# Performance work log

Measured on AMD Instinct MI355X. Metric: run time of the kernel, lower is better.

The kernel has to match this reference:

```python
import jax, jax.numpy as jnp
import numpy as np

B, T, IN, H, OUT = 128, 256, 1, 5000, 20


def setup_inputs() -> dict:
    key = jax.random.key(0)
    k1, k2, k3, k4, k5 = jax.random.split(key, 5)
    return {
        "x": jax.random.normal(k1, (B, T, IN), dtype=jnp.float32),
        "W_in": jax.random.normal(k2, (H, IN), dtype=jnp.float32) * (1.0 / np.sqrt(IN)),
        "b_in": jax.random.normal(k3, (H,), dtype=jnp.float32) * 0.01,
        "W_out": jax.random.normal(k4, (OUT, H), dtype=jnp.float32) * (1.0 / np.sqrt(H)),
        "b_out": jax.random.normal(k5, (OUT,), dtype=jnp.float32) * 0.01,
    }


def reference(x, W_in, b_in, W_out, b_out):
    # x: [B, T, IN]; recurrence: h_{t+1} = tanh(x_t @ W_in^T + b_in + h_t)
    batch = x.shape[0]
    hidden = W_in.shape[0]
    h0 = jnp.zeros((batch, hidden), dtype=x.dtype)
    xs = jnp.swapaxes(x, 0, 1)  # [T, B, IN] for scan over time

    def step(h, x_t):
        h_new = jnp.tanh(x_t @ W_in.T + b_in + h)
        return h_new, None

    h_final, _ = jax.lax.scan(step, h0, xs)
    logits = h_final @ W_out.T + b_out  # [B, OUT]
    return jax.nn.softmax(logits, axis=-1)
```

## Files before the change

kernel.cpp:

```cpp
#include <hip/hip_runtime.h>

#define T_STEPS 256
#define BATCH   128
#define HIDDEN  5000
#define NOUT    20
#define HB      256

__global__ __launch_bounds__(256, 8)
void rnn_recurrence(const float* __restrict__ x,
                    const float* __restrict__ W_in,
                    const float* __restrict__ b_in,
                    float* __restrict__ h_out) {
    __shared__ float xs[T_STEPS];
    const int hb  = blockIdx.x;
    const int b   = blockIdx.y;
    const int tid = threadIdx.x;

    xs[tid] = x[b * T_STEPS + tid];
    __syncthreads();

    const int hidx = hb * HB + tid;
    if (hidx < HIDDEN) {
        const float c     = 2.8853900817779268f;
        const float inv_c = 0.34657359027997264f;
        const float wc = W_in[hidx] * c;
        const float bc = b_in[hidx] * c;
        float hc = 0.0f;
        #pragma unroll 8
        for (int t = 0; t < T_STEPS; ++t) {
            float u = fmaf(xs[t], wc, hc + bc);
            float e = __builtin_amdgcn_exp2f(u);
            float r = __builtin_amdgcn_rcpf(e + 1.0f);
            hc = fmaf(-2.0f * c, r, c);
        }
        h_out[b * HIDDEN + hidx] = hc * inv_c;
    }
}

__global__ __launch_bounds__(256)
void head_softmax(const float* __restrict__ h,
                  const float* __restrict__ W_out,
                  const float* __restrict__ b_out,
                  float* __restrict__ out) {
    const int b   = blockIdx.x;
    const int tid = threadIdx.x;

    float acc[NOUT];
    #pragma unroll
    for (int o = 0; o < NOUT; ++o) acc[o] = 0.0f;

    for (int i = tid; i < HIDDEN; i += 256) {
        const float hv = h[b * HIDDEN + i];
        #pragma unroll
        for (int o = 0; o < NOUT; ++o)
            acc[o] = fmaf(hv, W_out[o * HIDDEN + i], acc[o]);
    }

    #pragma unroll
    for (int o = 0; o < NOUT; ++o) {
        #pragma unroll
        for (int s = 32; s > 0; s >>= 1)
            acc[o] += __shfl_down(acc[o], s, 64);
    }

    __shared__ float partial[4][NOUT];
    const int wid = tid >> 6, lane = tid & 63;
    if (lane == 0) {
        #pragma unroll
        for (int o = 0; o < NOUT; ++o) partial[wid][o] = acc[o];
    }
    __syncthreads();

    if (tid == 0) {
        float logits[NOUT];
        float m = -1e30f;
        #pragma unroll
        for (int o = 0; o < NOUT; ++o) {
            float v = partial[0][o] + partial[1][o] + partial[2][o]
                    + partial[3][o] + b_out[o];
            logits[o] = v;
            m = fmaxf(m, v);
        }
        float s = 0.0f;
        float e[NOUT];
        #pragma unroll
        for (int o = 0; o < NOUT; ++o) {
            e[o] = __builtin_amdgcn_exp2f((logits[o] - m) * 1.4426950408889634f);
            s += e[o];
        }
        const float inv = 1.0f / s;
        #pragma unroll
        for (int o = 0; o < NOUT; ++o) out[b * NOUT + o] = e[o] * inv;
    }
}

extern "C" void kernel_launch(void* const* d_in, const int* in_sizes, int n_in,
                              void* d_out, int out_size, void* d_ws, size_t ws_size,
                              hipStream_t stream) {
    const float* x     = (const float*)d_in[0];
    const float* W_in  = (const float*)d_in[1];
    const float* b_in  = (const float*)d_in[2];
    const float* W_out = (const float*)d_in[3];
    const float* b_out = (const float*)d_in[4];
    float* out  = (float*)d_out;
    float* h_ws = (float*)d_ws;

    dim3 grid1((HIDDEN + HB - 1) / HB, BATCH);
    rnn_recurrence<<<grid1, 256, 0, stream>>>(x, W_in, b_in, h_ws);
    head_softmax<<<BATCH, 256, 0, stream>>>(h_ws, W_out, b_out, out);
}
```

Before: 110.4 us.

## Process two hidden units per thread, fold bias into exp, vectorize head loads

Each thread now runs two independent recurrences, which gives more instruction-level parallelism to hide the exp2/rcp latency on the serial dependency chain and halves the grid. The bias is folded algebraically into a precomputed multiplier exp2(b*c), so the per-step add becomes part of an fma. The shared-memory staging of x is replaced by direct global (cached) reads. The head kernel uses float4 loads for h and W_out. Per-step precision may shift slightly because exp2(u)*K replaces exp2(u+bc), which can overflow differently for large arguments.

```diff
diff --git a/kernel.cpp b/kernel.cpp
--- a/kernel.cpp
+++ b/kernel.cpp
@@ -3,38 +3,47 @@
 #define T_STEPS 256
 #define BATCH   128
 #define HIDDEN  5000
+#define NHALF   2500
 #define NOUT    20
-#define HB      256
 
-__global__ __launch_bounds__(256, 8)
+__global__ __launch_bounds__(256)
 void rnn_recurrence(const float* __restrict__ x,
                     const float* __restrict__ W_in,
                     const float* __restrict__ b_in,
                     float* __restrict__ h_out) {
-    __shared__ float xs[T_STEPS];
-    const int hb  = blockIdx.x;
-    const int b   = blockIdx.y;
-    const int tid = threadIdx.x;
+    const int b  = blockIdx.y;
+    const int i0 = blockIdx.x * 256 + threadIdx.x;
+    if (i0 >= NHALF) return;
+    const int i1 = i0 + NHALF;
 
-    xs[tid] = x[b * T_STEPS + tid];
-    __syncthreads();
+    const float c     = 2.8853900817779268f;
+    const float inv_c = 0.34657359027997264f;
+    const float n2c   = -5.7707801635558537f;
 
-    const int hidx = hb * HB + tid;
-    if (hidx < HIDDEN) {
-        const float c     = 2.8853900817779268f;
-        const float inv_c = 0.34657359027997264f;
-        const float wc = W_in[hidx] * c;
-        const float bc = b_in[hidx] * c;
-        float hc = 0.0f;
-        #pragma unroll 8
-        for (int t = 0; t < T_STEPS; ++t) {
-            float u = fmaf(xs[t], wc, hc + bc);
-            float e = __builtin_amdgcn_exp2f(u);
-            float r = __builtin_amdgcn_rcpf(e + 1.0f);
-            hc = fmaf(-2.0f * c, r, c);
-        }
-        h_out[b * HIDDEN + hidx] = hc * inv_c;
+    const float wc0 = W_in[i0] * c;
+    const float wc1 = W_in[i1] * c;
+    const float K0  = __builtin_amdgcn_exp2f(b_in[i0] * c);
+    const float K1  = __builtin_amdgcn_exp2f(b_in[i1] * c);
+
+    const float* __restrict__ xrow = x + b * T_STEPS;
+
+    float hc0 = 0.0f, hc1 = 0.0f;
+    #pragma unroll 16
+    for (int t = 0; t < T_STEPS; ++t) {
+        const float xv = xrow[t];
+        float u0 = fmaf(xv, wc0, hc0);
+        float u1 = fmaf(xv, wc1, hc1);
+        float e0 = __builtin_amdgcn_exp2f(u0);
+        float e1 = __builtin_amdgcn_exp2f(u1);
+        float d0 = fmaf(e0, K0, 1.0f);
+        float d1 = fmaf(e1, K1, 1.0f);
+        float r0 = __builtin_amdgcn_rcpf(d0);
+        float r1 = __builtin_amdgcn_rcpf(d1);
+        hc0 = fmaf(r0, n2c, c);
+        hc1 = fmaf(r1, n2c, c);
     }
+    h_out[b * HIDDEN + i0] = hc0 * inv_c;
+    h_out[b * HIDDEN + i1] = hc1 * inv_c;
 }
 
 __global__ __launch_bounds__(256)
@@ -45,15 +54,23 @@
     const int b   = blockIdx.x;
     const int tid = threadIdx.x;
 
+    const float4* __restrict__ h4 = (const float4*)(h + b * HIDDEN);
+    const float4* __restrict__ w4 = (const float4*)W_out;
+
     float acc[NOUT];
     #pragma unroll
     for (int o = 0; o < NOUT; ++o) acc[o] = 0.0f;
 
-    for (int i = tid; i < HIDDEN; i += 256) {
-        const float hv = h[b * HIDDEN + i];
+    for (int i4 = tid; i4 < HIDDEN / 4; i4 += 256) {
+        const float4 hv = h4[i4];
         #pragma unroll
-        for (int o = 0; o < NOUT; ++o)
-            acc[o] = fmaf(hv, W_out[o * HIDDEN + i], acc[o]);
+        for (int o = 0; o < NOUT; ++o) {
+            const float4 wv = w4[o * (HIDDEN / 4) + i4];
+            acc[o] = fmaf(hv.x, wv.x, acc[o]);
+            acc[o] = fmaf(hv.y, wv.y, acc[o]);
+            acc[o] = fmaf(hv.z, wv.z, acc[o]);
+            acc[o] = fmaf(hv.w, wv.w, acc[o]);
+        }
     }
 
     #pragma unroll
@@ -105,7 +122,7 @@
     float* out  = (float*)d_out;
     float* h_ws = (float*)d_ws;
 
-    dim3 grid1((HIDDEN + HB - 1) / HB, BATCH);
+    dim3 grid1((NHALF + 255) / 256, BATCH);
     rnn_recurrence<<<grid1, 256, 0, stream>>>(x, W_in, b_in, h_ws);
     head_softmax<<<BATCH, 256, 0, stream>>>(h_ws, W_out, b_out, out);
 }
```

Result: faster. 102.1 us (-7.6%).
